# Kernel optimization log

Measured on AMD Instinct MI355X. Metric: run time of the kernel, lower is better.

The kernel has to match this reference:

```python
import jax, jax.numpy as jnp
import numpy as np

NUM_MODELS = 64
OUT_F = 256
IN_F = 256
B = 32768
F0 = 2
F1 = 2


def setup_inputs() -> dict:
    key = jax.random.key(0)
    k1, k2, k3, k4 = jax.random.split(key, 4)
    sqrt_k = float(np.sqrt(1.0 / NUM_MODELS))
    weights = 2 * sqrt_k * jax.random.uniform(k1, (NUM_MODELS, OUT_F, IN_F), dtype=jnp.float32) - sqrt_k
    biases = 2 * sqrt_k * jax.random.uniform(k2, (NUM_MODELS, OUT_F), dtype=jnp.float32) - sqrt_k
    inputs = jax.random.normal(k3, (B, IN_F // F1), dtype=jnp.float32)
    indices = jax.random.randint(k4, (B,), 0, NUM_MODELS, dtype=jnp.int64)
    return {"inputs": inputs, "weights": weights, "biases": biases,
            "indices": indices, "factor0": F0, "factor1": F1}


def reference(inputs, weights, biases, indices, factor0, factor1):
    out_sub = weights.shape[1] // factor0
    in_sub = weights.shape[2] // factor1
    # Gather per-sample weight slices: (B, out_sub, in_sub)
    subweight = weights[indices, :out_sub, :in_sub]
    subbias = biases[indices, :out_sub]  # (B, out_sub)
    # Batched matvec + bias
    return jnp.einsum('boi,bi->bo', subweight, inputs) + subbias
```

## Files before the change

### kernel.cpp

```cpp
#include <hip/hip_runtime.h>
#include <hip/hip_bf16.h>

#define NMODELS 64
#define NB      32768
#define INF     256
#define OUTF    256
#define INS     128
#define OUTS    128
#define TILE_M  64
#define NT      8
#define NSB     128
#define POISON  0xAAAAAAAAu

typedef unsigned int u32;
typedef unsigned short u16;
using bf16x8  = __attribute__((ext_vector_type(8))) short;
using f32x4   = __attribute__((ext_vector_type(4))) float;
using float4v = __attribute__((ext_vector_type(4))) float;
using short8v = __attribute__((ext_vector_type(8))) short;

__device__ __forceinline__ u16 f2bf(float f) {
    union { float fv; u32 u; } v; v.fv = f;
    u32 u = v.u;
    u += 0x7fffu + ((u >> 16) & 1u);
    return (u16)(u >> 16);
}

__global__ __launch_bounds__(256) void k_scat(const int* __restrict__ idx,
                                              u32* __restrict__ cursors,
                                              int* __restrict__ perm) {
    __shared__ int h[NMODELS];
    __shared__ int base[NMODELS];
    const int t = threadIdx.x;
    const int i = blockIdx.x * 256 + t;
    const int m = idx[i];
    if (t < NMODELS) h[t] = 0;
    __syncthreads();
    const int r = atomicAdd(&h[m], 1);
    __syncthreads();
    if (t < NMODELS && h[t] != 0)
        base[t] = (int)(atomicAdd(&cursors[t], (u32)h[t]) - POISON);
    __syncthreads();
    perm[(m << 10) + base[m] + r] = i;
}

__global__ __launch_bounds__(256, 2) void k_gemm(const float* __restrict__ x,
                                                 const float* __restrict__ w,
                                                 const float* __restrict__ bias,
                                                 const u32* __restrict__ cursors,
                                                 const int* __restrict__ perm,
                                                 float* __restrict__ out) {
    __shared__ __align__(16) u16 Ws[OUTS * 128];
    const int m    = blockIdx.x;
    const int t    = threadIdx.x;
    const int wave = t >> 6;
    const int lane = t & 63;
    const int quad = lane >> 4;
    const int lr   = lane & 15;

    const float* wsrc = w + (size_t)m * (OUTF * INF);
    float4v wv[16];
    #pragma unroll
    for (int it = 0; it < 8; ++it) {
        const int cid = (it << 8) + t;
        const int row = cid >> 4;
        const int c   = cid & 15;
        const float* src = wsrc + row * INF + (c << 3);
        wv[2 * it]     = *(const float4v*)(src);
        wv[2 * it + 1] = *(const float4v*)(src + 4);
    }

    const int pbase = m << 10;
    int tile = blockIdx.y;
    int row  = tile * TILE_M + wave * 16 + lr;
    int p    = perm[pbase + row];
    const int cnt = (int)(cursors[m] - POISON);

    #pragma unroll
    for (int it = 0; it < 8; ++it) {
        const int cid = (it << 8) + t;
        const int row2 = cid >> 4;
        const int c    = cid & 15;
        short8v s;
        s[0]=(short)f2bf(wv[2*it].x);   s[1]=(short)f2bf(wv[2*it].y);
        s[2]=(short)f2bf(wv[2*it].z);   s[3]=(short)f2bf(wv[2*it].w);
        s[4]=(short)f2bf(wv[2*it+1].x); s[5]=(short)f2bf(wv[2*it+1].y);
        s[6]=(short)f2bf(wv[2*it+1].z); s[7]=(short)f2bf(wv[2*it+1].w);
        *(short8v*)&Ws[(row2 << 7) + ((c ^ (row2 & 15)) << 3)] = s;
    }

    int  pidx = p & (NB - 1);
    bool v    = row < cnt;
    const float* xr = x + (size_t)pidx * INS + quad * 8;
    float4v xa[8];
    #pragma unroll
    for (int k0 = 0; k0 < 4; ++k0) {
        xa[2 * k0]     = *(const float4v*)(xr + k0 * 32);
        xa[2 * k0 + 1] = *(const float4v*)(xr + k0 * 32 + 4);
    }
    float4v bv4[8];
    #pragma unroll
    for (int nt = 0; nt < 8; ++nt)
        bv4[nt] = *(const float4v*)(bias + m * OUTF + nt * 16 + quad * 4);

    int xoff[4];
    #pragma unroll
    for (int k0 = 0; k0 < 4; ++k0) xoff[k0] = ((k0 * 4 + quad) ^ lr) * 8;
    const int rowbase = lr * 128;

    __syncthreads();

    for (;;) {
        bf16x8 xb[4];
        #pragma unroll
        for (int k0 = 0; k0 < 4; ++k0) {
            bf16x8 a;
            a[0] = (short)f2bf(xa[2*k0].x);   a[1] = (short)f2bf(xa[2*k0].y);
            a[2] = (short)f2bf(xa[2*k0].z);   a[3] = (short)f2bf(xa[2*k0].w);
            a[4] = (short)f2bf(xa[2*k0+1].x); a[5] = (short)f2bf(xa[2*k0+1].y);
            a[6] = (short)f2bf(xa[2*k0+1].z); a[7] = (short)f2bf(xa[2*k0+1].w);
            xb[k0] = a;
        }
        f32x4 acc[8];
        #pragma unroll
        for (int nt = 0; nt < 8; ++nt) acc[nt] = (f32x4){0.f, 0.f, 0.f, 0.f};
        #pragma unroll
        for (int k0 = 0; k0 < 4; ++k0) {
            #pragma unroll
            for (int nt = 0; nt < 8; ++nt) {
                bf16x8 wfr = *(const bf16x8*)&Ws[nt * 2048 + rowbase + xoff[k0]];
                acc[nt] = __builtin_amdgcn_mfma_f32_16x16x32_bf16(wfr, xb[k0], acc[nt], 0, 0, 0);
            }
        }
        const int  curpi = pidx;
        const bool curv  = v;
        const int  ntile = tile + NT;
        const bool more  = (ntile * TILE_M < cnt);
        if (more) {
            row  = ntile * TILE_M + wave * 16 + lr;
            p    = perm[pbase + row];
            pidx = p & (NB - 1);
            v    = row < cnt;
            const float* xr2 = x + (size_t)pidx * INS + quad * 8;
            #pragma unroll
            for (int k0 = 0; k0 < 4; ++k0) {
                xa[2 * k0]     = *(const float4v*)(xr2 + k0 * 32);
                xa[2 * k0 + 1] = *(const float4v*)(xr2 + k0 * 32 + 4);
            }
        }
        if (curv) {
            float* orow = out + (size_t)curpi * OUTS + quad * 4;
            #pragma unroll
            for (int nt = 0; nt < 8; ++nt)
                *(float4v*)(orow + nt * 16) = acc[nt] + bv4[nt];
        }
        if (!more) break;
        tile = ntile;
    }
}

extern "C" void kernel_launch(void* const* d_in, const int* in_sizes, int n_in,
                              void* d_out, int out_size, void* d_ws, size_t ws_size,
                              hipStream_t stream) {
    const float* x    = (const float*)d_in[0];
    const float* w    = (const float*)d_in[1];
    const float* bias = (const float*)d_in[2];
    const int*   idx  = (const int*)d_in[3];
    float* out = (float*)d_out;

    int* ws      = (int*)d_ws;
    u32* cursors = (u32*)ws;
    int* perm    = ws + 64;

    k_scat<<<dim3(NSB),        dim3(256), 0, stream>>>(idx, cursors, perm);
    k_gemm<<<dim3(NMODELS, NT), dim3(256), 0, stream>>>(x, w, bias, cursors, perm, out);
}
```

Baseline: 91.90 us.

## Fuse scatter histogram kernel into GEMM kernel with grid-wide spin barrier

Merges the index scatter kernel into the grouped GEMM kernel. The first 128 blocks each bucket 256 indices into the perm array and bump a global done counter. All blocks then spin on that counter before reading perm, and the weight loads and bf16 conversion overlap the scatter phase. This removes one kernel launch and the gap between kernels, but it relies on all 512 blocks being co-resident to avoid deadlock and on the workspace being poisoned to the expected initial value.

```diff
diff --git a/kernel.cpp b/kernel.cpp
--- a/kernel.cpp
+++ b/kernel.cpp
@@ -9,7 +9,6 @@
 #define OUTS    128
 #define TILE_M  64
 #define NT      8
-#define NSB     128
 #define POISON  0xAAAAAAAAu
 
 typedef unsigned int u32;
@@ -26,30 +25,14 @@
     return (u16)(u >> 16);
 }
 
-__global__ __launch_bounds__(256) void k_scat(const int* __restrict__ idx,
-                                              u32* __restrict__ cursors,
-                                              int* __restrict__ perm) {
-    __shared__ int h[NMODELS];
-    __shared__ int base[NMODELS];
-    const int t = threadIdx.x;
-    const int i = blockIdx.x * 256 + t;
-    const int m = idx[i];
-    if (t < NMODELS) h[t] = 0;
-    __syncthreads();
-    const int r = atomicAdd(&h[m], 1);
-    __syncthreads();
-    if (t < NMODELS && h[t] != 0)
-        base[t] = (int)(atomicAdd(&cursors[t], (u32)h[t]) - POISON);
-    __syncthreads();
-    perm[(m << 10) + base[m] + r] = i;
-}
-
-__global__ __launch_bounds__(256, 2) void k_gemm(const float* __restrict__ x,
-                                                 const float* __restrict__ w,
-                                                 const float* __restrict__ bias,
-                                                 const u32* __restrict__ cursors,
-                                                 const int* __restrict__ perm,
-                                                 float* __restrict__ out) {
+__global__ __launch_bounds__(256, 2) void k_fused(const float* __restrict__ x,
+                                                  const float* __restrict__ w,
+                                                  const float* __restrict__ bias,
+                                                  const int* __restrict__ idx,
+                                                  u32* __restrict__ cursors,
+                                                  int* __restrict__ perm,
+                                                  u32* __restrict__ done,
+                                                  float* __restrict__ out) {
     __shared__ __align__(16) u16 Ws[OUTS * 128];
     const int m    = blockIdx.x;
     const int t    = threadIdx.x;
@@ -70,15 +53,30 @@
         wv[2 * it + 1] = *(const float4v*)(src + 4);
     }
 
-    const int pbase = m << 10;
-    int tile = blockIdx.y;
-    int row  = tile * TILE_M + wave * 16 + lr;
-    int p    = perm[pbase + row];
-    const int cnt = (int)(cursors[m] - POISON);
+    if (blockIdx.y < 2) {
+        int* hist = (int*)Ws;
+        int* base = (int*)Ws + 64;
+        const int seg = m + (blockIdx.y << 6);
+        const int i   = (seg << 8) + t;
+        const int mi  = idx[i];
+        if (t < NMODELS) hist[t] = 0;
+        __syncthreads();
+        const int r = atomicAdd(&hist[mi], 1);
+        __syncthreads();
+        if (t < NMODELS && hist[t] != 0)
+            base[t] = (int)(atomicAdd(&cursors[t], (u32)hist[t]) - POISON);
+        __syncthreads();
+        perm[(mi << 10) + base[mi] + r] = i;
+        __syncthreads();
+        if (t == 0) {
+            __threadfence();
+            __hip_atomic_fetch_add(done, 1u, __ATOMIC_RELEASE, __HIP_MEMORY_SCOPE_AGENT);
+        }
+    }
 
     #pragma unroll
     for (int it = 0; it < 8; ++it) {
-        const int cid = (it << 8) + t;
+        const int cid  = (it << 8) + t;
         const int row2 = cid >> 4;
         const int c    = cid & 15;
         short8v s;
@@ -89,8 +87,21 @@
         *(short8v*)&Ws[(row2 << 7) + ((c ^ (row2 & 15)) << 3)] = s;
     }
 
+    if (t == 0) {
+        while ((u32)(__hip_atomic_load(done, __ATOMIC_ACQUIRE, __HIP_MEMORY_SCOPE_AGENT)
+                     - POISON) < 128u)
+            __builtin_amdgcn_s_sleep(1);
+    }
+    __syncthreads();
+
+    const int pbase = m << 10;
+    int tile = blockIdx.y;
+    int row  = tile * TILE_M + wave * 16 + lr;
+    int p    = perm[pbase + row];
+    const int cnt = (int)(cursors[m] - POISON);
     int  pidx = p & (NB - 1);
     bool v    = row < cnt;
+
     const float* xr = x + (size_t)pidx * INS + quad * 8;
     float4v xa[8];
     #pragma unroll
@@ -107,8 +118,6 @@
     #pragma unroll
     for (int k0 = 0; k0 < 4; ++k0) xoff[k0] = ((k0 * 4 + quad) ^ lr) * 8;
     const int rowbase = lr * 128;
-
-    __syncthreads();
 
     for (;;) {
         bf16x8 xb[4];
@@ -171,7 +180,8 @@
     int* ws      = (int*)d_ws;
     u32* cursors = (u32*)ws;
     int* perm    = ws + 64;
+    u32* done    = (u32*)(ws + 64 + 65536);
 
-    k_scat<<<dim3(NSB),        dim3(256), 0, stream>>>(idx, cursors, perm);
-    k_gemm<<<dim3(NMODELS, NT), dim3(256), 0, stream>>>(x, w, bias, cursors, perm, out);
+    k_fused<<<dim3(NMODELS, NT), dim3(256), 0, stream>>>(x, w, bias, idx,
+                                                         cursors, perm, done, out);
 }
```

After: 117.4 us. 1.28x slower.

## Fuse index bucketing into GEMM kernel via per-block segment scan

Applied to the files above, without the earlier changes.

Removes the separate scatter kernel and global permutation buffer. Each block (model, segment) scans a 4096-entry slice of the index array, collects matching sample ids into shared memory with an LDS atomic, then runs the same MFMA matvec loop over those samples. This saves one kernel launch and the global atomics and perm round trip. In exchange, every block reads its whole index slice, and the selection is capped at 768 entries per block, so an unusually skewed index distribution would silently drop samples. Sample order within a block also becomes nondeterministic.

```diff
diff --git a/kernel.cpp b/kernel.cpp
--- a/kernel.cpp
+++ b/kernel.cpp
@@ -8,8 +8,8 @@
 #define INS     128
 #define OUTS    128
 #define TILE_M  64
-#define NT      8
-#define NSB     128
+#define NSEG    8
+#define SELCAP  768
 #define POISON  0xAAAAAAAAu
 
 typedef unsigned int u32;
@@ -18,6 +18,7 @@
 using f32x4   = __attribute__((ext_vector_type(4))) float;
 using float4v = __attribute__((ext_vector_type(4))) float;
 using short8v = __attribute__((ext_vector_type(8))) short;
+using int4v   = __attribute__((ext_vector_type(4))) int;
 
 __device__ __forceinline__ u16 f2bf(float f) {
     union { float fv; u32 u; } v; v.fv = f;
@@ -26,32 +27,16 @@
     return (u16)(u >> 16);
 }
 
-__global__ __launch_bounds__(256) void k_scat(const int* __restrict__ idx,
-                                              u32* __restrict__ cursors,
-                                              int* __restrict__ perm) {
-    __shared__ int h[NMODELS];
-    __shared__ int base[NMODELS];
-    const int t = threadIdx.x;
-    const int i = blockIdx.x * 256 + t;
-    const int m = idx[i];
-    if (t < NMODELS) h[t] = 0;
-    __syncthreads();
-    const int r = atomicAdd(&h[m], 1);
-    __syncthreads();
-    if (t < NMODELS && h[t] != 0)
-        base[t] = (int)(atomicAdd(&cursors[t], (u32)h[t]) - POISON);
-    __syncthreads();
-    perm[(m << 10) + base[m] + r] = i;
-}
-
-__global__ __launch_bounds__(256, 2) void k_gemm(const float* __restrict__ x,
-                                                 const float* __restrict__ w,
-                                                 const float* __restrict__ bias,
-                                                 const u32* __restrict__ cursors,
-                                                 const int* __restrict__ perm,
-                                                 float* __restrict__ out) {
+__global__ __launch_bounds__(256, 2) void k_one(const float* __restrict__ x,
+                                                const float* __restrict__ w,
+                                                const float* __restrict__ bias,
+                                                const int* __restrict__ idx,
+                                                float* __restrict__ out) {
     __shared__ __align__(16) u16 Ws[OUTS * 128];
+    __shared__ int sel[SELCAP];
+    __shared__ int scnt;
     const int m    = blockIdx.x;
+    const int y    = blockIdx.y;
     const int t    = threadIdx.x;
     const int wave = t >> 6;
     const int lane = t & 63;
@@ -70,15 +55,20 @@
         wv[2 * it + 1] = *(const float4v*)(src + 4);
     }
 
-    const int pbase = m << 10;
-    int tile = blockIdx.y;
-    int row  = tile * TILE_M + wave * 16 + lr;
-    int p    = perm[pbase + row];
-    const int cnt = (int)(cursors[m] - POISON);
+    const int* iseg = idx + (y << 12);
+    int4v iv[4];
+    #pragma unroll
+    for (int r = 0; r < 4; ++r)
+        iv[r] = *(const int4v*)(iseg + (r << 10) + (t << 2));
+    float4v bv4[8];
+    #pragma unroll
+    for (int nt = 0; nt < 8; ++nt)
+        bv4[nt] = *(const float4v*)(bias + m * OUTF + nt * 16 + quad * 4);
+    if (t == 0) scnt = 0;
 
     #pragma unroll
     for (int it = 0; it < 8; ++it) {
-        const int cid = (it << 8) + t;
+        const int cid  = (it << 8) + t;
         const int row2 = cid >> 4;
         const int c    = cid & 15;
         short8v s;
@@ -89,8 +79,32 @@
         *(short8v*)&Ws[(row2 << 7) + ((c ^ (row2 & 15)) << 3)] = s;
     }
 
-    int  pidx = p & (NB - 1);
-    bool v    = row < cnt;
+    __syncthreads();
+
+    #pragma unroll
+    for (int r = 0; r < 4; ++r) {
+        #pragma unroll
+        for (int j = 0; j < 4; ++j) {
+            if (iv[r][j] == m) {
+                const int pos = atomicAdd(&scnt, 1);
+                if (pos < SELCAP) sel[pos] = (y << 12) + (r << 10) + (t << 2) + j;
+            }
+        }
+    }
+    __syncthreads();
+
+    const int cnt = scnt < SELCAP ? scnt : SELCAP;
+    if (cnt == 0) return;
+
+    int xoff[4];
+    #pragma unroll
+    for (int k0 = 0; k0 < 4; ++k0) xoff[k0] = ((k0 * 4 + quad) ^ lr) * 8;
+    const int rowbase = lr * 128;
+
+    int tile = 0;
+    int row  = wave * 16 + lr;
+    bool v   = row < cnt;
+    int pidx = sel[v ? row : 0];
     const float* xr = x + (size_t)pidx * INS + quad * 8;
     float4v xa[8];
     #pragma unroll
@@ -98,17 +112,6 @@
         xa[2 * k0]     = *(const float4v*)(xr + k0 * 32);
         xa[2 * k0 + 1] = *(const float4v*)(xr + k0 * 32 + 4);
     }
-    float4v bv4[8];
-    #pragma unroll
-    for (int nt = 0; nt < 8; ++nt)
-        bv4[nt] = *(const float4v*)(bias + m * OUTF + nt * 16 + quad * 4);
-
-    int xoff[4];
-    #pragma unroll
-    for (int k0 = 0; k0 < 4; ++k0) xoff[k0] = ((k0 * 4 + quad) ^ lr) * 8;
-    const int rowbase = lr * 128;
-
-    __syncthreads();
 
     for (;;) {
         bf16x8 xb[4];
@@ -134,13 +137,12 @@
         }
         const int  curpi = pidx;
         const bool curv  = v;
-        const int  ntile = tile + NT;
+        const int  ntile = tile + 1;
         const bool more  = (ntile * TILE_M < cnt);
         if (more) {
             row  = ntile * TILE_M + wave * 16 + lr;
-            p    = perm[pbase + row];
-            pidx = p & (NB - 1);
             v    = row < cnt;
+            pidx = sel[v ? row : 0];
             const float* xr2 = x + (size_t)pidx * INS + quad * 8;
             #pragma unroll
             for (int k0 = 0; k0 < 4; ++k0) {
@@ -167,11 +169,7 @@
     const float* bias = (const float*)d_in[2];
     const int*   idx  = (const int*)d_in[3];
     float* out = (float*)d_out;
+    (void)d_ws; (void)ws_size;
 
-    int* ws      = (int*)d_ws;
-    u32* cursors = (u32*)ws;
-    int* perm    = ws + 64;
-
-    k_scat<<<dim3(NSB),        dim3(256), 0, stream>>>(idx, cursors, perm);
-    k_gemm<<<dim3(NMODELS, NT), dim3(256), 0, stream>>>(x, w, bias, cursors, perm, out);
+    k_one<<<dim3(NMODELS, NSEG), dim3(256), 0, stream>>>(x, w, bias, idx, out);
 }
```

Result: no change. 90.25 us (-1.8%).
